# Optimization experiments

Measured on AMD Instinct MI355X. Metric: run time of the kernel, lower is better.

## Reference

```python
import jax, jax.numpy as jnp
import numpy as np

DIM_IN = 1024
DIM_OUT = 1024
CTX = 2048


def setup_inputs() -> dict:
    key = jax.random.key(0)
    k_x, k_q, k_k, k_v = jax.random.split(key, 4)
    x = jax.random.normal(k_x, (4, CTX, DIM_IN), dtype=jnp.float32)
    # nn.Linear default init ~ U(-1/sqrt(fan_in), 1/sqrt(fan_in)); scale doesn't matter for correctness
    s = 1.0 / np.sqrt(DIM_IN)
    Wq = jax.random.uniform(k_q, (DIM_IN, DIM_OUT), jnp.float32, -s, s)
    Wk = jax.random.uniform(k_k, (DIM_IN, DIM_OUT), jnp.float32, -s, s)
    Wv = jax.random.uniform(k_v, (DIM_IN, DIM_OUT), jnp.float32, -s, s)
    return {"x": x, "Wq": Wq, "Wk": Wk, "Wv": Wv}


def reference(x, Wq, Wk, Wv):
    # x: [B, T, D_in]; W*: [D_in, D_out]
    b, t, _ = x.shape
    q = jnp.einsum('btd,de->bte', x, Wq)
    k = jnp.einsum('btd,de,->bte', x, Wk, jnp.float32(1.0)) if False else jnp.einsum('btd,de->bte', x, Wk)
    v = jnp.einsum('btd,de->bte', x, Wv)
    scores = jnp.einsum('bqe,bke->bqk', q, k)  # [B, T, T]
    causal = jnp.tril(jnp.ones((t, t), dtype=bool))  # True where allowed
    scores = jnp.where(causal, scores, -jnp.inf)
    weights = jax.nn.softmax(scores / jnp.sqrt(jnp.float32(k.shape[-1])), axis=-1)
    # dropout p=0.0 -> identity
    return jnp.einsum('bqk,bke->bqe', weights, v)
```

## Files before the change

kernel.cpp:

```cpp
#include <hip/hip_runtime.h>


using f32x4 = __attribute__((ext_vector_type(4))) float;
using s16x8 = __attribute__((ext_vector_type(8))) short;

#define CTX 2048
#define DIM 1024
#define NB 4

__device__ __forceinline__ short f2bf(float f) {
  union { float f; unsigned u; } v; v.f = f;
  unsigned r = (v.u + 0x7fffu + ((v.u >> 16) & 1u)) >> 16;
  return (short)r;
}

__device__ __forceinline__ void async16(const void* g, void* l) {
  __builtin_amdgcn_global_load_lds(
      (const __attribute__((address_space(1))) void*)g,
      (__attribute__((address_space(3))) void*)l, 16, 0, 0);
}


__global__ __launch_bounds__(256) void cvt_x(const float* __restrict__ in,
                                             short* __restrict__ out, long n8) {
  long i = (long)blockIdx.x * 256 + threadIdx.x;
  if (i >= n8) return;
  const float4* p = (const float4*)in;
  float4 a = p[i * 2], b = p[i * 2 + 1];
  short o[8];
  o[0] = f2bf(a.x); o[1] = f2bf(a.y); o[2] = f2bf(a.z); o[3] = f2bf(a.w);
  o[4] = f2bf(b.x); o[5] = f2bf(b.y); o[6] = f2bf(b.z); o[7] = f2bf(b.w);
  *(int4*)&out[i * 8] = *(int4*)o;
}

__global__ __launch_bounds__(256) void cvt_wT(const float* __restrict__ Wq,
                                              const float* __restrict__ Wk,
                                              const float* __restrict__ Wv,
                                              short* __restrict__ WT) {
  int z = blockIdx.z;
  const float* W = (z == 0) ? Wq : (z == 1) ? Wk : Wv;
  short* o = WT + (long)z * DIM * DIM;
  __shared__ float t[32][33];
  int n0 = blockIdx.x * 32, k0 = blockIdx.y * 32;
  int tx = threadIdx.x, ty = threadIdx.y;
  #pragma unroll
  for (int j = 0; j < 4; ++j)
    t[ty + j * 8][tx] = W[(long)(k0 + ty + j * 8) * DIM + n0 + tx];
  __syncthreads();
  #pragma unroll
  for (int j = 0; j < 4; ++j)
    o[(long)(n0 + ty + j * 8) * DIM + k0 + tx] = f2bf(t[tx][ty + j * 8]);
}

template <int MODE, bool CSKIP, bool KLIM>
__global__ __launch_bounds__(256) void gemm_bt(const short* __restrict__ A,
                                               const short* __restrict__ B,
                                               void* __restrict__ Cout,
                                               int M, int N, int K,
                                               long sA, long sB, long sC, int ldc) {
  const int bx = blockIdx.x, by = blockIdx.y, bz = blockIdx.z;
  if (CSKIP && by > bx) return;
  const short* Ab = A + bz * sA + (long)bx * 128 * K;
  const short* Bb = B + bz * sB + (long)by * 128 * K;
  __shared__ short As[2][128 * 32];
  __shared__ short Bs[2][128 * 32];
  const int tid = threadIdx.x;
  const int lane = tid & 63, wid = tid >> 6;
  const int wr = wid >> 1, wc = wid & 1;
  const int frow = lane & 15, kgrp = lane >> 4;

  f32x4 acc[4][4];
  const f32x4 zero = {0.f, 0.f, 0.f, 0.f};
  #pragma unroll
  for (int m = 0; m < 4; ++m)
    #pragma unroll
    for (int n = 0; n < 4; ++n) acc[m][n] = zero;

  int kt_end = K >> 5;
  if (KLIM) { int lim = (bx + 1) << 2; if (lim < kt_end) kt_end = lim; }

  const int e0 = wid * 512 + lane * 8;
  const int er = e0 >> 5, ec = e0 & 31;

  #pragma unroll
  for (int p = 0; p < 2; ++p) {
    const int e = e0 + (p << 11);
    const int r = er + (p << 6);
    async16(Ab + (long)r * K + ec, &As[0][e]);
    async16(Bb + (long)r * K + ec, &Bs[0][e]);
  }
  asm volatile("s_waitcnt vmcnt(0)");
  __syncthreads();

  int cur = 0;
  for (int kt = 0; kt < kt_end; ++kt) {
    if (kt + 1 < kt_end) {
      const int k0n = (kt + 1) << 5;
      #pragma unroll
      for (int p = 0; p < 2; ++p) {
        const int e = e0 + (p << 11);
        const int r = er + (p << 6);
        async16(Ab + (long)r * K + (k0n + ec), &As[cur ^ 1][e]);
        async16(Bb + (long)r * K + (k0n + ec), &Bs[cur ^ 1][e]);
      }
    }

    s16x8 af[4], bfr[4];
    #pragma unroll
    for (int m = 0; m < 4; ++m)
      af[m] = *(const s16x8*)&As[cur][((wr << 6) + (m << 4) + frow) * 32 + (kgrp << 3)];
    #pragma unroll
    for (int n = 0; n < 4; ++n)
      bfr[n] = *(const s16x8*)&Bs[cur][((wc << 6) + (n << 4) + frow) * 32 + (kgrp << 3)];
    #pragma unroll
    for (int m = 0; m < 4; ++m)
      #pragma unroll
      for (int n = 0; n < 4; ++n)
        acc[m][n] = __builtin_amdgcn_mfma_f32_16x16x32_bf16(af[m], bfr[n], acc[m][n], 0, 0, 0);

    asm volatile("s_waitcnt vmcnt(0)");
    __syncthreads();
    cur ^= 1;
  }

  const int row0 = (bx << 7) + (wr << 6);
  const int col0 = (by << 7) + (wc << 6);
  #pragma unroll
  for (int m = 0; m < 4; ++m) {
    #pragma unroll
    for (int n = 0; n < 4; ++n) {
      #pragma unroll
      for (int r = 0; r < 4; ++r) {
        const int row = row0 + (m << 4) + (kgrp << 2) + r;
        const int col = col0 + (n << 4) + frow;
        const float v = acc[m][n][r];
        if (MODE == 2) {
          ((_Float16*)Cout)[bz * sC + (long)row * ldc + col] = (_Float16)v;
        } else if (MODE == 3) {
          ((float*)Cout)[bz * sC + (long)row * ldc + col] = v;
        } else {
          const long QK = (long)NB * CTX * DIM;
          long off;
          if (col < 2048) {
            off = (long)(col >> 10) * QK + (long)row * DIM + (col & 1023);
          } else {
            off = 2 * QK + (long)(row >> 11) * ((long)DIM * CTX) +
                  (long)(col - 2048) * CTX + (row & (CTX - 1));
          }
          ((short*)Cout)[off] = f2bf(v);
        }
      }
    }
  }
}

__global__ __launch_bounds__(256) void softmax_causal(void* __restrict__ Sbuf) {
  const int r = blockIdx.x, b = blockIdx.y;
  const long base = (long)b * CTX * CTX + (long)r * CTX;
  _Float16* S = (_Float16*)Sbuf + base;
  short* P = (short*)Sbuf + base;
  const int tid = threadIdx.x;
  const int lane = tid & 63, wid = tid >> 6;
  const int c0 = tid * 8;
  const float scale = 0.03125f;

  _Float16 h[8];
  *(int4*)h = *(const int4*)&S[c0];
  float v[8];
  float m = -INFINITY;
  #pragma unroll
  for (int j = 0; j < 8; ++j) {
    v[j] = (c0 + j <= r) ? (float)h[j] * scale : -INFINITY;
    m = fmaxf(m, v[j]);
  }
  #pragma unroll
  for (int off = 32; off >= 1; off >>= 1) m = fmaxf(m, __shfl_xor(m, off));
  __shared__ float redm[4], reds[4];
  if (lane == 0) redm[wid] = m;
  __syncthreads();
  m = fmaxf(fmaxf(redm[0], redm[1]), fmaxf(redm[2], redm[3]));

  float p[8];
  float s = 0.f;
  #pragma unroll
  for (int j = 0; j < 8; ++j) {
    p[j] = exp2f((v[j] - m) * 1.44269504f);
    s += p[j];
  }
  #pragma unroll
  for (int off = 32; off >= 1; off >>= 1) s += __shfl_xor(s, off);
  if (lane == 0) reds[wid] = s;
  __syncthreads();
  s = reds[0] + reds[1] + reds[2] + reds[3];
  const float inv = 1.0f / s;

  short o[8];
  #pragma unroll
  for (int j = 0; j < 8; ++j) o[j] = f2bf(p[j] * inv);
  *(int4*)&P[c0] = *(int4*)o;
}

extern "C" void kernel_launch(void* const* d_in, const int* in_sizes, int n_in,
                              void* d_out, int out_size, void* d_ws, size_t ws_size,
                              hipStream_t stream) {
  (void)in_sizes; (void)n_in; (void)out_size; (void)ws_size;
  const float* x  = (const float*)d_in[0];
  const float* Wq = (const float*)d_in[1];
  const float* Wk = (const float*)d_in[2];
  const float* Wv = (const float*)d_in[3];

  const long MB = 1024 * 1024;
  char* ws = (char*)d_ws;
  short* xb = (short*)(ws + 0);
  short* WT = (short*)(ws + 16 * MB);
  short* Qb = (short*)(ws + 24 * MB);
  short* Kb = (short*)(ws + 40 * MB);
  short* Vt = (short*)(ws + 56 * MB);
  void*  S  = (void*)(ws + 72 * MB);

  cvt_x<<<4096, 256, 0, stream>>>(x, xb, (long)NB * CTX * DIM / 8);
  cvt_wT<<<dim3(32, 32, 3), dim3(32, 8), 0, stream>>>(Wq, Wk, Wv, WT);
  gemm_bt<4, false, false><<<dim3(64, 24, 1), 256, 0, stream>>>(
      xb, WT, Qb, NB * CTX, 3 * DIM, DIM, 0, 0, 0, DIM);
  gemm_bt<2, true, false><<<dim3(16, 16, NB), 256, 0, stream>>>(
      Qb, Kb, S, CTX, CTX, DIM, (long)CTX * DIM, (long)CTX * DIM, (long)CTX * CTX, CTX);
  softmax_causal<<<dim3(CTX, NB), 256, 0, stream>>>(S);
  gemm_bt<3, false, true><<<dim3(16, 8, NB), 256, 0, stream>>>(
      (short*)S, Vt, d_out, CTX, DIM, CTX, (long)CTX * CTX, (long)DIM * CTX, (long)CTX * DIM, DIM);
}
```

Measured before the change: 285.0 us.

## Triple-buffer GEMM loads, reverse causal block order, skip masked softmax traffic

The GEMM moves from double to triple-buffered async LDS loads, prefetching two k-tiles ahead with a partial vmcnt wait and a single barrier per iteration, so global loads overlap more with MFMA work. For the PV GEMM, blocks are launched in reverse row order so the longest causal blocks start first, which evens out the tail. The softmax skips loading fully masked columns and writes probabilities only up to the 128-column boundary that the PV GEMM reads, cutting memory traffic. The extra stage raises LDS use per block, which may lower occupancy.

```diff
diff --git a/kernel.cpp b/kernel.cpp
--- a/kernel.cpp
+++ b/kernel.cpp
@@ -58,12 +58,13 @@
                                                void* __restrict__ Cout,
                                                int M, int N, int K,
                                                long sA, long sB, long sC, int ldc) {
-  const int bx = blockIdx.x, by = blockIdx.y, bz = blockIdx.z;
+  const int bx = KLIM ? ((int)gridDim.x - 1 - (int)blockIdx.x) : (int)blockIdx.x;
+  const int by = blockIdx.y, bz = blockIdx.z;
   if (CSKIP && by > bx) return;
   const short* Ab = A + bz * sA + (long)bx * 128 * K;
   const short* Bb = B + bz * sB + (long)by * 128 * K;
-  __shared__ short As[2][128 * 32];
-  __shared__ short Bs[2][128 * 32];
+  __shared__ short As[3][128 * 32];
+  __shared__ short Bs[3][128 * 32];
   const int tid = threadIdx.x;
   const int lane = tid & 63, wid = tid >> 6;
   const int wr = wid >> 1, wc = wid & 1;
@@ -83,25 +84,32 @@
   const int er = e0 >> 5, ec = e0 & 31;
 
   #pragma unroll
-  for (int p = 0; p < 2; ++p) {
-    const int e = e0 + (p << 11);
-    const int r = er + (p << 6);
-    async16(Ab + (long)r * K + ec, &As[0][e]);
-    async16(Bb + (long)r * K + ec, &Bs[0][e]);
-  }
-  asm volatile("s_waitcnt vmcnt(0)");
-  __syncthreads();
-
-  int cur = 0;
+  for (int t = 0; t < 2; ++t) {
+    const int k0 = t << 5;
+    #pragma unroll
+    for (int p = 0; p < 2; ++p) {
+      const int e = e0 + (p << 11);
+      const int r = er + (p << 6);
+      async16(Ab + (long)r * K + (k0 + ec), &As[t][e]);
+      async16(Bb + (long)r * K + (k0 + ec), &Bs[t][e]);
+    }
+  }
+
+  int cur = 0, stg = 2;
   for (int kt = 0; kt < kt_end; ++kt) {
-    if (kt + 1 < kt_end) {
-      const int k0n = (kt + 1) << 5;
+    if (kt + 1 < kt_end) asm volatile("s_waitcnt vmcnt(4)" ::: "memory");
+    else                 asm volatile("s_waitcnt vmcnt(0)" ::: "memory");
+    __builtin_amdgcn_s_barrier();
+    asm volatile("" ::: "memory");
+
+    if (kt + 2 < kt_end) {
+      const int k0n = (kt + 2) << 5;
       #pragma unroll
       for (int p = 0; p < 2; ++p) {
         const int e = e0 + (p << 11);
         const int r = er + (p << 6);
-        async16(Ab + (long)r * K + (k0n + ec), &As[cur ^ 1][e]);
-        async16(Bb + (long)r * K + (k0n + ec), &Bs[cur ^ 1][e]);
+        async16(Ab + (long)r * K + (k0n + ec), &As[stg][e]);
+        async16(Bb + (long)r * K + (k0n + ec), &Bs[stg][e]);
       }
     }
 
@@ -118,9 +126,8 @@
       for (int n = 0; n < 4; ++n)
         acc[m][n] = __builtin_amdgcn_mfma_f32_16x16x32_bf16(af[m], bfr[n], acc[m][n], 0, 0, 0);
 
-    asm volatile("s_waitcnt vmcnt(0)");
-    __syncthreads();
-    cur ^= 1;
+    cur = (cur == 2) ? 0 : cur + 1;
+    stg = (stg == 2) ? 0 : stg + 1;
   }
 
   const int row0 = (bx << 7) + (wr << 6);
@@ -162,17 +169,23 @@
   const int tid = threadIdx.x;
   const int lane = tid & 63, wid = tid >> 6;
   const int c0 = tid * 8;
+  const int ncol = ((r >> 7) + 1) << 7;
   const float scale = 0.03125f;
 
-  _Float16 h[8];
-  *(int4*)h = *(const int4*)&S[c0];
   float v[8];
+  if (c0 <= r) {
+    _Float16 h[8];
+    *(int4*)h = *(const int4*)&S[c0];
+    #pragma unroll
+    for (int j = 0; j < 8; ++j)
+      v[j] = (c0 + j <= r) ? (float)h[j] * scale : -INFINITY;
+  } else {
+    #pragma unroll
+    for (int j = 0; j < 8; ++j) v[j] = -INFINITY;
+  }
   float m = -INFINITY;
   #pragma unroll
-  for (int j = 0; j < 8; ++j) {
-    v[j] = (c0 + j <= r) ? (float)h[j] * scale : -INFINITY;
-    m = fmaxf(m, v[j]);
-  }
+  for (int j = 0; j < 8; ++j) m = fmaxf(m, v[j]);
   #pragma unroll
   for (int off = 32; off >= 1; off >>= 1) m = fmaxf(m, __shfl_xor(m, off));
   __shared__ float redm[4], reds[4];
@@ -194,10 +207,12 @@
   s = reds[0] + reds[1] + reds[2] + reds[3];
   const float inv = 1.0f / s;
 
-  short o[8];
-  #pragma unroll
-  for (int j = 0; j < 8; ++j) o[j] = f2bf(p[j] * inv);
-  *(int4*)&P[c0] = *(int4*)o;
+  if (c0 < ncol) {
+    short o[8];
+    #pragma unroll
+    for (int j = 0; j < 8; ++j) o[j] = f2bf(p[j] * inv);
+    *(int4*)&P[c0] = *(int4*)o;
+  }
 }
 
 extern "C" void kernel_launch(void* const* d_in, const int* in_sizes, int n_in,
```

Result: no change. 284.9 us (-0.0%).
